# Performance work log

Measured on AMD Instinct MI355X. Metric: run time of the kernel, lower is better.

## Reference

```python
import jax, jax.numpy as jnp
import numpy as np

B, S, T, D, H_HEADS = 2, 2048, 2048, 1024, 16
HD = D // H_HEADS
EPS = 1e-5


def _ln(x, g, b):
    m = jnp.mean(x, axis=-1, keepdims=True)
    v = jnp.mean(jnp.square(x - m), axis=-1, keepdims=True)
    return g * (x - m) * jax.lax.rsqrt(v + EPS) + b


def _mha(xq, xkv, Wq, bq, Wk, bk, Wv, bv, Wo, bo, causal):
    Bq, Lq, _ = xq.shape
    Lk = xkv.shape[1]
    q = (xq @ Wq + bq).reshape(Bq, Lq, H_HEADS, HD)
    k = (xkv @ Wk + bk).reshape(Bq, Lk, H_HEADS, HD)
    v = (xkv @ Wv + bv).reshape(Bq, Lk, H_HEADS, HD)
    scores = jnp.einsum('bqhd,bkhd->bhqk', q, k) / jnp.sqrt(jnp.asarray(HD, q.dtype))
    if causal:
        mask = jnp.tril(jnp.ones((Lq, Lk), dtype=bool))
        scores = jnp.where(mask, scores, jnp.asarray(-1e9, scores.dtype))
    p = jax.nn.softmax(scores, axis=-1)
    o = jnp.einsum('bhqk,bkhd->bqhd', p, v).reshape(Bq, Lq, D)
    return o @ Wo + bo


def setup_inputs() -> dict:
    key = jax.random.key(0)
    ks = jax.random.split(key, 24)
    s = 0.02
    def w(i):
        return jax.random.normal(ks[i], (D, D), jnp.float32) * s
    inp = {
        'S0': jax.random.normal(ks[20], (B, S, D), jnp.float32),
        'H': jax.random.normal(ks[21], (B, T, D), jnp.float32),
        'Wq1': w(0), 'bq1': jnp.zeros((D,)), 'Wk1': w(1), 'bk1': jnp.zeros((D,)),
        'Wv1': w(2), 'bv1': jnp.zeros((D,)), 'Wo1': w(3), 'bo1': jnp.zeros((D,)),
        'ln1_g': jnp.ones((D,)), 'ln1_b': jnp.zeros((D,)),
        'Wq2': w(4), 'bq2': jnp.zeros((D,)), 'Wk2': w(5), 'bk2': jnp.zeros((D,)),
        'Wv2': w(6), 'bv2': jnp.zeros((D,)), 'Wo2': w(7), 'bo2': jnp.zeros((D,)),
        'ln2_g': jnp.ones((D,)), 'ln2_b': jnp.zeros((D,)),
        'Wf': w(8), 'bf': jnp.zeros((D,)),
        'ln3_g': jnp.ones((D,)), 'ln3_b': jnp.zeros((D,)),
    }
    return inp


def reference(S0, H, Wq1, bq1, Wk1, bk1, Wv1, bv1, Wo1, bo1, ln1_g, ln1_b,
              Wq2, bq2, Wk2, bk2, Wv2, bv2, Wo2, bo2, ln2_g, ln2_b,
              Wf, bf, ln3_g, ln3_b):
    # masked (causal) self-attention + add&norm
    a1 = _mha(S0, S0, Wq1, bq1, Wk1, bk1, Wv1, bv1, Wo1, bo1, causal=True)
    S1 = _ln(S0 + a1, ln1_g, ln1_b)
    # cross-attention over encoder output H + add&norm
    a2 = _mha(S1, H, Wq2, bq2, Wk2, bk2, Wv2, bv2, Wo2, bo2, causal=False)
    S2 = _ln(S1 + a2, ln2_g, ln2_b)
    # FFN (single Linear) + add&norm
    S3 = _ln(S2 + (S2 @ Wf + bf), ln3_g, ln3_b)
    return S3
```

## Files before the change

### kernel.cpp

```cpp
#include <hip/hip_runtime.h>
#include <hip/hip_bf16.h>
#include <cstdint>
#include <cstddef>


#define D_DIM 1024
#define SEQ   2048
#define NHEAD 16
#define HDIM  64
#define MROWS 4096

typedef __attribute__((ext_vector_type(8)))  short bf16x8;
typedef __attribute__((ext_vector_type(4)))  float f32x4;
typedef __attribute__((ext_vector_type(16))) float f32x16;
typedef __attribute__((ext_vector_type(4)))  unsigned int u32x4;

static __device__ __forceinline__ short f2bf(float x) {
    __hip_bfloat16 h = __float2bfloat16(x);
    return *reinterpret_cast<short*>(&h);
}

static __device__ __forceinline__ unsigned int cvtpk(float lo, float hi2) {
    unsigned int r;
    asm("v_cvt_pk_bf16_f32 %0, %1, %2" : "=v"(r) : "v"(lo), "v"(hi2));
    return r;
}

#define GLOAD_LDS16(g, l)                                                     \
    __builtin_amdgcn_global_load_lds(                                         \
        (const __attribute__((address_space(1))) unsigned int*)(g),           \
        (__attribute__((address_space(3))) unsigned int*)(l), 16, 0, 0)

struct WPtrs { const float* p[9]; };

__global__ __launch_bounds__(256) void transpose_conv_kernel(
    WPtrs wp, short* __restrict__ Wt)
{
    __shared__ float tl[64][65];
    const int t = threadIdx.x;
    const float* src = wp.p[blockIdx.z];
    short* dst = Wt + (size_t)blockIdx.z * D_DIM * D_DIM;
    const int r0 = blockIdx.x * 64;
    const int c0 = blockIdx.y * 64;
    #pragma unroll
    for (int i = 0; i < 4; ++i) {
        int row = i * 16 + (t >> 4);
        int col = (t & 15) * 4;
        float4 v = *(const float4*)(src + (size_t)(r0 + row) * D_DIM + c0 + col);
        tl[row][col + 0] = v.x; tl[row][col + 1] = v.y;
        tl[row][col + 2] = v.z; tl[row][col + 3] = v.w;
    }
    __syncthreads();
    #pragma unroll
    for (int i = 0; i < 4; ++i) {
        int nrow = i * 16 + (t >> 4);
        int kcol = (t & 15) * 4;
        ushort4 o;
        o.x = (unsigned short)f2bf(tl[kcol + 0][nrow]);
        o.y = (unsigned short)f2bf(tl[kcol + 1][nrow]);
        o.z = (unsigned short)f2bf(tl[kcol + 2][nrow]);
        o.w = (unsigned short)f2bf(tl[kcol + 3][nrow]);
        *(ushort4*)(dst + (size_t)(c0 + nrow) * D_DIM + r0 + kcol) = o;
    }
}

__global__ __launch_bounds__(256) void conv2_kernel(
    const float* __restrict__ s0, const float* __restrict__ hx,
    short* __restrict__ d0, short* __restrict__ d1)
{
    const bool second = blockIdx.x >= 2048;
    const float* src = second ? hx : s0;
    short* dst = second ? d1 : d0;
    size_t i = ((size_t)(blockIdx.x - (second ? 2048 : 0)) * 256 + threadIdx.x) * 8;
    float4 a = *(const float4*)(src + i);
    float4 b = *(const float4*)(src + i + 4);
    bf16x8 o;
    o[0] = f2bf(a.x); o[1] = f2bf(a.y); o[2] = f2bf(a.z); o[3] = f2bf(a.w);
    o[4] = f2bf(b.x); o[5] = f2bf(b.y); o[6] = f2bf(b.z); o[7] = f2bf(b.w);
    *(bf16x8*)(dst + i) = o;
}

__global__ __launch_bounds__(256) void bias_concat_kernel(
    const float* __restrict__ bq1, const float* __restrict__ bk1,
    const float* __restrict__ bv1, const float* __restrict__ bk2,
    const float* __restrict__ bv2, float* __restrict__ cb1,
    float* __restrict__ cb2)
{
    const int i = blockIdx.x * 256 + threadIdx.x;
    if      (i < 1024) cb1[i] = bq1[i];
    else if (i < 2048) cb1[i] = bk1[i - 1024];
    else if (i < 3072) cb1[i] = bv1[i - 2048];
    else if (i < 4096) cb2[i - 3072] = bk2[i - 3072];
    else               cb2[i - 3072] = bv2[i - 4096];
}

#define GEMM_CORE(A_, Bt_)                                                    \
    __shared__ short As[128 * 32];                                            \
    __shared__ short Bs[128 * 32];                                            \
    const int t = threadIdx.x;                                                \
    const int wave = t >> 6, lane = t & 63;                                   \
    const int wm = wave >> 1, wn = wave & 1;                                  \
    const int m0 = blockIdx.x * 128, n0 = blockIdx.y * 128;                   \
    const int l15 = lane & 15, l4 = lane >> 4;                                \
    const int lrow = lane >> 2, lcol = (lane & 3) * 8;                        \
    f32x4 acc[4][4] = {};                                                     \
    for (int k0 = 0; k0 < D_DIM; k0 += 32) {                                  \
        __syncthreads();                                                      \
        _Pragma("unroll")                                                     \
        for (int c = 0; c < 2; ++c) {                                         \
            int chunk = wave + c * 4;                                         \
            int row = chunk * 16 + lrow;                                      \
            GLOAD_LDS16(A_  + (size_t)(m0 + row) * D_DIM + k0 + lcol,         \
                        As + chunk * 512 + lane * 8);                         \
            GLOAD_LDS16(Bt_ + (size_t)(n0 + row) * D_DIM + k0 + lcol,         \
                        Bs + chunk * 512 + lane * 8);                         \
        }                                                                     \
        __syncthreads();                                                      \
        bf16x8 af[4], bfr[4];                                                 \
        const int kq = l4 * 8;                                                \
        _Pragma("unroll")                                                     \
        for (int i = 0; i < 4; ++i)                                           \
            af[i] = *(const bf16x8*)&As[(wm * 64 + i * 16 + l15) * 32 + kq];  \
        _Pragma("unroll")                                                     \
        for (int j = 0; j < 4; ++j)                                           \
            bfr[j] = *(const bf16x8*)&Bs[(wn * 64 + j * 16 + l15) * 32 + kq]; \
        _Pragma("unroll")                                                     \
        for (int i = 0; i < 4; ++i)                                           \
            _Pragma("unroll")                                                 \
            for (int j = 0; j < 4; ++j)                                       \
                acc[i][j] = __builtin_amdgcn_mfma_f32_16x16x32_bf16(          \
                    af[i], bfr[j], acc[i][j], 0, 0, 0);                       \
    }                                                                         \
    const int rbase = m0 + wm * 64;                                           \
    const int cbase = n0 + wn * 64;

__global__ __launch_bounds__(256) void gemm_resid_kernel(
    const short* __restrict__ A, const short* __restrict__ Bt,
    const float* __restrict__ bias, const float* __restrict__ resid,
    float* __restrict__ Cout)
{
    __shared__ short As[128 * 32];
    __shared__ short Bs[64 * 32];
    const int t = threadIdx.x;
    const int wave = t >> 6, lane = t & 63;
    const int wm = wave >> 1, wn = wave & 1;
    const int m0 = blockIdx.x * 128, n0 = blockIdx.y * 64;
    const int l15 = lane & 15, l4 = lane >> 4;
    const int lrow = lane >> 2, lcol = (lane & 3) * 8;
    f32x4 acc[4][2] = {};
    for (int k0 = 0; k0 < D_DIM; k0 += 32) {
        __syncthreads();
        #pragma unroll
        for (int c = 0; c < 2; ++c) {
            int chunk = wave + c * 4;
            int row = chunk * 16 + lrow;
            GLOAD_LDS16(A + (size_t)(m0 + row) * D_DIM + k0 + lcol,
                        As + chunk * 512 + lane * 8);
        }
        {
            int row = wave * 16 + lrow;
            GLOAD_LDS16(Bt + (size_t)(n0 + row) * D_DIM + k0 + lcol,
                        Bs + wave * 512 + lane * 8);
        }
        __syncthreads();
        bf16x8 af[4], bfr[2];
        const int kq = l4 * 8;
        #pragma unroll
        for (int i = 0; i < 4; ++i)
            af[i] = *(const bf16x8*)&As[(wm * 64 + i * 16 + l15) * 32 + kq];
        #pragma unroll
        for (int j = 0; j < 2; ++j)
            bfr[j] = *(const bf16x8*)&Bs[(wn * 32 + j * 16 + l15) * 32 + kq];
        #pragma unroll
        for (int i = 0; i < 4; ++i)
            #pragma unroll
            for (int j = 0; j < 2; ++j)
                acc[i][j] = __builtin_amdgcn_mfma_f32_16x16x32_bf16(
                    af[i], bfr[j], acc[i][j], 0, 0, 0);
    }
    const int rbase = m0 + wm * 64;
    const int cbase = n0 + wn * 32;
    float bv[2];
    #pragma unroll
    for (int j = 0; j < 2; ++j) bv[j] = bias[cbase + j * 16 + l15];
    #pragma unroll
    for (int i = 0; i < 4; ++i) {
        #pragma unroll
        for (int r = 0; r < 4; ++r) {
            const int grow = rbase + i * 16 + l4 * 4 + r;
            #pragma unroll
            for (int j = 0; j < 2; ++j) {
                const int gcol = cbase + j * 16 + l15;
                float v = acc[i][j][r] + bv[j]
                        + resid[(size_t)grow * D_DIM + gcol];
                Cout[(size_t)grow * D_DIM + gcol] = v;
            }
        }
    }
}

__global__ __launch_bounds__(256) void gemm_qkv_kernel(
    const short* __restrict__ A, const short* __restrict__ Bt,
    const float* __restrict__ bias,
    short* __restrict__ Qh, short* __restrict__ Kh, short* __restrict__ Vh,
    int col0, float qscale)
{
    GEMM_CORE(A, Bt)
    float bv[4];
    #pragma unroll
    for (int j = 0; j < 4; ++j) bv[j] = bias[cbase + j * 16 + l15];
    #pragma unroll
    for (int i = 0; i < 4; ++i) {
        #pragma unroll
        for (int r = 0; r < 4; ++r) {
            const int grow = rbase + i * 16 + l4 * 4 + r;
            const int b = grow >> 11, s = grow & 2047;
            #pragma unroll
            for (int j = 0; j < 4; ++j) {
                const int vcol = col0 + cbase + j * 16 + l15;
                float v = acc[i][j][r] + bv[j];
                if (vcol < 1024) v *= qscale;
                short* dst = (vcol < 1024) ? Qh : ((vcol < 2048) ? Kh : Vh);
                const int h = (vcol >> 6) & 15, hd = vcol & 63;
                dst[((size_t)(b * 16 + h) * SEQ + s) * HDIM + hd] = f2bf(v);
            }
        }
    }
}

template<bool CAUSAL>
__global__ __launch_bounds__(256, 2) void attn_mfma_kernel(
    const short* __restrict__ Qh, const short* __restrict__ Kh,
    const short* __restrict__ Vh, short* __restrict__ O)
{
    __shared__ short Ks[2][128 * 64];
    __shared__ short Vt[2][64 * 128];

    const int t = threadIdx.x, wave = t >> 6, lane = t & 63;
    const int q_own = lane & 31, hi = lane >> 5;
    const int id = blockIdx.x;
    const int bh = ((id & 7) << 2) | ((id >> 3) & 3);
    const int qsel = id >> 5;
    const int b = bh >> 4, h = bh & 15;
    const short* Qp = Qh + (size_t)bh * SEQ * HDIM;
    const short* Kp = Kh + (size_t)bh * SEQ * HDIM;
    const short* Vp = Vh + (size_t)bh * SEQ * HDIM;
    short* Op = O + (size_t)b * SEQ * D_DIM + h * HDIM;

    const int ksrc = (t & 7) ^ ((t >> 3) & 7);
    const int vr2 = (t & 31) * 2, vg = (t >> 5) * 8;

    bf16x8 va0, vb0, va1, vb1;

    #define K_GLL(kb, buf)                                                    \
        do {                                                                  \
            _Pragma("unroll")                                                 \
            for (int c = 0; c < 4; ++c) {                                     \
                const int row = c * 32 + (t >> 3);                            \
                GLOAD_LDS16(Kp + (size_t)((kb) + row) * HDIM + ksrc * 8,      \
                            &Ks[buf][(c * 256 + t) * 8]);                     \
            }                                                                 \
        } while (0)

    #define V_LOAD(kb)                                                        \
        do {                                                                  \
            va0 = *(const bf16x8*)(Vp + (size_t)((kb) + vr2) * HDIM + vg);    \
            vb0 = *(const bf16x8*)(Vp + (size_t)((kb) + vr2 + 1) * HDIM + vg);\
            va1 = *(const bf16x8*)(Vp + (size_t)((kb) + 64 + vr2) * HDIM + vg);\
            vb1 = *(const bf16x8*)(Vp + (size_t)((kb) + 64 + vr2 + 1) * HDIM + vg);\
        } while (0)

    #define V_WRITE(buf)                                                      \
        do {                                                                  \
            _Pragma("unroll")                                                 \
            for (int j = 0; j < 8; ++j) {                                     \
                const int hd = vg + j;                                        \
                unsigned int p0 = ((unsigned int)(unsigned short)vb0[j] << 16)\
                                | (unsigned short)va0[j];                     \
                *(unsigned int*)&Vt[buf][(hd * 128 + vr2) ^ ((hd & 7) << 3)] = p0;\
                unsigned int p1 = ((unsigned int)(unsigned short)vb1[j] << 16)\
                                | (unsigned short)va1[j];                     \
                *(unsigned int*)&Vt[buf][(hd * 128 + 64 + vr2) ^ ((hd & 7) << 3)] = p1;\
            }                                                                 \
        } while (0)

    const int npm = CAUSAL ? 2 : 1;
    for (int pm = 0; pm < npm; ++pm) {
        const int qt = CAUSAL ? (pm == 0 ? qsel : 15 - qsel) : qsel;
        const int q0 = qt * 128;
        const int qw = q0 + wave * 32;

        bf16x8 qf[4];
        #pragma unroll
        for (int s = 0; s < 4; ++s)
            qf[s] = *(const bf16x8*)(Qp + (size_t)(qw + q_own) * HDIM
                                     + s * 16 + hi * 8);

        f32x16 oacc[2] = {};
        float m_ = -3e38f, l_ = 0.f;
        const int nkt = CAUSAL ? (qt + 1) : (SEQ / 128);

        if (pm) __syncthreads();

        K_GLL(0, 0);
        V_LOAD(0);
        V_WRITE(0);
        __syncthreads();

        for (int kt = 0; kt < nkt; ++kt) {
            const int cur = kt & 1, nxt = cur ^ 1;
            const int kbase = kt * 128;
            const bool have_next = (kt + 1 < nkt);

            if (have_next) {
                K_GLL(kbase + 128, nxt);
                V_LOAD(kbase + 128);
            }

            f32x16 sc[4] = {};
            __builtin_amdgcn_s_setprio(1);
            #pragma unroll
            for (int kt2 = 0; kt2 < 4; ++kt2) {
                const int krow = kt2 * 32 + q_own;
                #pragma unroll
                for (int s = 0; s < 4; ++s) {
                    bf16x8 kf = *(const bf16x8*)&Ks[cur]
                        [(krow * 64 + s * 16 + hi * 8) ^ ((krow & 7) << 3)];
                    sc[kt2] = __builtin_amdgcn_mfma_f32_32x32x16_bf16(
                        kf, qf[s], sc[kt2], 0, 0, 0);
                }
            }
            __builtin_amdgcn_s_setprio(0);

            if (CAUSAL && (kbase + 127 > qw)) {
                #pragma unroll
                for (int kt2 = 0; kt2 < 4; ++kt2)
                    #pragma unroll
                    for (int rr = 0; rr < 16; ++rr) {
                        const int k = kbase + kt2 * 32
                                    + (rr & 3) + 8 * (rr >> 2) + 4 * hi;
                        if (k > qw + q_own) sc[kt2][rr] = -1e30f;
                    }
            }

            float pmax = sc[0][0];
            #pragma unroll
            for (int kt2 = 0; kt2 < 4; ++kt2) {
                float p0 = fmaxf(fmaxf(sc[kt2][0], sc[kt2][1]),
                                 fmaxf(sc[kt2][2], sc[kt2][3]));
                float p1 = fmaxf(fmaxf(sc[kt2][4], sc[kt2][5]),
                                 fmaxf(sc[kt2][6], sc[kt2][7]));
                float p2 = fmaxf(fmaxf(sc[kt2][8], sc[kt2][9]),
                                 fmaxf(sc[kt2][10], sc[kt2][11]));
                float p3 = fmaxf(fmaxf(sc[kt2][12], sc[kt2][13]),
                                 fmaxf(sc[kt2][14], sc[kt2][15]));
                float q01 = fmaxf(p0, p1), q23 = fmaxf(p2, p3);
                pmax = (kt2 == 0) ? fmaxf(q01, q23)
                                  : fmaxf(pmax, fmaxf(q01, q23));
            }
            pmax = fmaxf(pmax, __shfl_xor(pmax, 32));

            if (!__all(pmax - m_ <= 8.0f)) {
                const float mnew = fmaxf(m_, pmax);
                const float corr = exp2f(m_ - mnew);
                l_ *= corr;
                #pragma unroll
                for (int ht = 0; ht < 2; ++ht)
                    #pragma unroll
                    for (int rr = 0; rr < 16; ++rr)
                        oacc[ht][rr] *= corr;
                m_ = mnew;
            }

            float s_own = 0.f;
            #pragma unroll
            for (int kt2 = 0; kt2 < 4; ++kt2) {
                float t0 = 0.f, t1 = 0.f, t2 = 0.f, t3 = 0.f;
                #pragma unroll
                for (int rr = 0; rr < 4; ++rr) {
                    float a = exp2f(sc[kt2][rr]      - m_);
                    float b2 = exp2f(sc[kt2][4 + rr]  - m_);
                    float c = exp2f(sc[kt2][8 + rr]  - m_);
                    float d = exp2f(sc[kt2][12 + rr] - m_);
                    sc[kt2][rr] = a;      t0 += a;
                    sc[kt2][4 + rr] = b2; t1 += b2;
                    sc[kt2][8 + rr] = c;  t2 += c;
                    sc[kt2][12 + rr] = d; t3 += d;
                }
                s_own += (t0 + t1) + (t2 + t3);
            }
            l_ += s_own + __shfl_xor(s_own, 32);

            u32x4 paw[8];
            #pragma unroll
            for (int kt2 = 0; kt2 < 4; ++kt2) {
                unsigned int w0a = cvtpk(sc[kt2][0],  sc[kt2][1]);
                unsigned int w0b = cvtpk(sc[kt2][2],  sc[kt2][3]);
                unsigned int w1a = cvtpk(sc[kt2][4],  sc[kt2][5]);
                unsigned int w1b = cvtpk(sc[kt2][6],  sc[kt2][7]);
                unsigned int w2a = cvtpk(sc[kt2][8],  sc[kt2][9]);
                unsigned int w2b = cvtpk(sc[kt2][10], sc[kt2][11]);
                unsigned int w3a = cvtpk(sc[kt2][12], sc[kt2][13]);
                unsigned int w3b = cvtpk(sc[kt2][14], sc[kt2][15]);
                asm("v_permlane32_swap_b32 %0, %1" : "+v"(w0a), "+v"(w1a));
                asm("v_permlane32_swap_b32 %0, %1" : "+v"(w0b), "+v"(w1b));
                asm("v_permlane32_swap_b32 %0, %1" : "+v"(w2a), "+v"(w3a));
                asm("v_permlane32_swap_b32 %0, %1" : "+v"(w2b), "+v"(w3b));
                paw[kt2 * 2 + 0][0] = w0a; paw[kt2 * 2 + 0][1] = w0b;
                paw[kt2 * 2 + 0][2] = w1a; paw[kt2 * 2 + 0][3] = w1b;
                paw[kt2 * 2 + 1][0] = w2a; paw[kt2 * 2 + 1][1] = w2b;
                paw[kt2 * 2 + 1][2] = w3a; paw[kt2 * 2 + 1][3] = w3b;
            }

            __builtin_amdgcn_s_setprio(1);
            #pragma unroll
            for (int ht = 0; ht < 2; ++ht) {
                const int vrow = ht * 32 + q_own;
                #pragma unroll
                for (int ks = 0; ks < 8; ++ks) {
                    bf16x8 vf = *(const bf16x8*)&Vt[cur]
                        [(vrow * 128 + ks * 16 + hi * 8) ^ ((vrow & 7) << 3)];
                    union { u32x4 u; bf16x8 bv8; } pc;
                    pc.u = paw[ks];
                    oacc[ht] = __builtin_amdgcn_mfma_f32_32x32x16_bf16(
                        vf, pc.bv8, oacc[ht], 0, 0, 0);
                }
            }
            __builtin_amdgcn_s_setprio(0);

            if (have_next) {
                V_WRITE(nxt);
                __syncthreads();
            }
        }

        const float inv = 1.0f / l_;
        const int grow = qw + q_own;
        #pragma unroll
        for (int ht = 0; ht < 2; ++ht)
            #pragma unroll
            for (int j = 0; j < 4; ++j) {
                ushort4 o;
                o.x = (unsigned short)f2bf(oacc[ht][4 * j + 0] * inv);
                o.y = (unsigned short)f2bf(oacc[ht][4 * j + 1] * inv);
                o.z = (unsigned short)f2bf(oacc[ht][4 * j + 2] * inv);
                o.w = (unsigned short)f2bf(oacc[ht][4 * j + 3] * inv);
                *(ushort4*)&Op[(size_t)grow * D_DIM + ht * 32 + 8 * j + 4 * hi] = o;
            }
    }
    #undef K_GLL
    #undef V_LOAD
    #undef V_WRITE
}

__global__ __launch_bounds__(256) void ln_kernel(
    const float* __restrict__ X, const float* __restrict__ g,
    const float* __restrict__ bb, float* __restrict__ outf,
    short* __restrict__ outb)
{
    const int row = blockIdx.x;
    const int t = threadIdx.x;
    const float* x = X + (size_t)row * D_DIM;
    float4 v = *(const float4*)(x + (t << 2));
    float s  = v.x + v.y + v.z + v.w;
    float sq = v.x * v.x + v.y * v.y + v.z * v.z + v.w * v.w;
    #pragma unroll
    for (int off = 1; off < 64; off <<= 1) {
        s  += __shfl_xor(s, off);
        sq += __shfl_xor(sq, off);
    }
    __shared__ float ss[4], ssq[4];
    const int wid = t >> 6, lane = t & 63;
    if (lane == 0) { ss[wid] = s; ssq[wid] = sq; }
    __syncthreads();
    s  = ss[0] + ss[1] + ss[2] + ss[3];
    sq = ssq[0] + ssq[1] + ssq[2] + ssq[3];
    const float mean = s * (1.0f / 1024.0f);
    const float var  = sq * (1.0f / 1024.0f) - mean * mean;
    const float inv  = rsqrtf(var + 1e-5f);
    float4 gv = *(const float4*)(g  + (t << 2));
    float4 bv = *(const float4*)(bb + (t << 2));
    float4 o;
    o.x = gv.x * (v.x - mean) * inv + bv.x;
    o.y = gv.y * (v.y - mean) * inv + bv.y;
    o.z = gv.z * (v.z - mean) * inv + bv.z;
    o.w = gv.w * (v.w - mean) * inv + bv.w;
    if (outf) *(float4*)(outf + (size_t)row * D_DIM + (t << 2)) = o;
    if (outb) {
        ushort4 ob;
        ob.x = (unsigned short)f2bf(o.x); ob.y = (unsigned short)f2bf(o.y);
        ob.z = (unsigned short)f2bf(o.z); ob.w = (unsigned short)f2bf(o.w);
        *(ushort4*)(outb + (size_t)row * D_DIM + (t << 2)) = ob;
    }
}

extern "C" void kernel_launch(void* const* d_in, const int* in_sizes, int n_in,
                              void* d_out, int out_size, void* d_ws, size_t ws_size,
                              hipStream_t stream)
{
    (void)in_sizes; (void)n_in; (void)out_size; (void)ws_size;
    const float* S0f = (const float*)d_in[0];
    const float* Hf  = (const float*)d_in[1];
    const float* bq1 = (const float*)d_in[3];
    const float* bk1 = (const float*)d_in[5];
    const float* bv1 = (const float*)d_in[7];
    const float* bo1 = (const float*)d_in[9];
    const float* g1  = (const float*)d_in[10]; const float* b1 = (const float*)d_in[11];
    const float* bq2 = (const float*)d_in[13];
    const float* bk2 = (const float*)d_in[15];
    const float* bv2 = (const float*)d_in[17];
    const float* bo2 = (const float*)d_in[19];
    const float* g2  = (const float*)d_in[20]; const float* b2 = (const float*)d_in[21];
    const float* bff = (const float*)d_in[23];
    const float* g3  = (const float*)d_in[24]; const float* b3 = (const float*)d_in[25];

    char* ws = (char*)d_ws;
    size_t off = 0;
    auto alloc = [&](size_t bytes) { char* p = ws + off; off += (bytes + 255) & ~(size_t)255; return p; };
    short* Wt   = (short*)alloc((size_t)9 * D_DIM * D_DIM * 2);
    short* bS0  = (short*)alloc((size_t)MROWS * D_DIM * 2);
    short* bH   = (short*)alloc((size_t)MROWS * D_DIM * 2);
    short* Qhb  = (short*)alloc((size_t)MROWS * D_DIM * 2);
    short* Khb  = (short*)alloc((size_t)MROWS * D_DIM * 2);
    short* Vhb  = (short*)alloc((size_t)MROWS * D_DIM * 2);
    short* bAO  = (short*)alloc((size_t)MROWS * D_DIM * 2);
    float* X    = (float*)alloc((size_t)MROWS * D_DIM * 4);
    short* bSx  = (short*)alloc((size_t)MROWS * D_DIM * 2);
    float* cb1  = (float*)alloc(3072 * 4);
    float* cb2  = (float*)alloc(2048 * 4);

    const size_t WSTRIDE = (size_t)D_DIM * D_DIM;
    const float QSCALE = 0.125f * 1.44269504088896f;

    WPtrs wp;
    wp.p[0] = (const float*)d_in[2];
    wp.p[1] = (const float*)d_in[4];
    wp.p[2] = (const float*)d_in[6];
    wp.p[3] = (const float*)d_in[8];
    wp.p[4] = (const float*)d_in[12];
    wp.p[5] = (const float*)d_in[14];
    wp.p[6] = (const float*)d_in[16];
    wp.p[7] = (const float*)d_in[18];
    wp.p[8] = (const float*)d_in[22];
    transpose_conv_kernel<<<dim3(16, 16, 9), 256, 0, stream>>>(wp, Wt);

    conv2_kernel<<<4096, 256, 0, stream>>>(S0f, Hf, bS0, bH);
    bias_concat_kernel<<<20, 256, 0, stream>>>(bq1, bk1, bv1, bk2, bv2, cb1, cb2);

    const dim3 blk(256);
    const dim3 attn_grid_c(256);
    const dim3 attn_grid_f(512);
    const dim3 resid_grid(32, 16);

    gemm_qkv_kernel<<<dim3(32, 24), blk, 0, stream>>>(
        bS0, Wt, cb1, Qhb, Khb, Vhb, 0, QSCALE);
    attn_mfma_kernel<true><<<attn_grid_c, blk, 0, stream>>>(Qhb, Khb, Vhb, bAO);
    gemm_resid_kernel<<<resid_grid, blk, 0, stream>>>(
        bAO, Wt + 3 * WSTRIDE, bo1, S0f, X);
    ln_kernel<<<MROWS, blk, 0, stream>>>(X, g1, b1, X, bSx);

    gemm_qkv_kernel<<<dim3(32, 8), blk, 0, stream>>>(
        bSx, Wt + 4 * WSTRIDE, bq2, Qhb, Khb, Vhb, 0, QSCALE);
    gemm_qkv_kernel<<<dim3(32, 16), blk, 0, stream>>>(
        bH, Wt + 5 * WSTRIDE, cb2, Qhb, Khb, Vhb, 1024, QSCALE);
    attn_mfma_kernel<false><<<attn_grid_f, blk, 0, stream>>>(Qhb, Khb, Vhb, bAO);
    gemm_resid_kernel<<<resid_grid, blk, 0, stream>>>(
        bAO, Wt + 7 * WSTRIDE, bo2, X, X);
    ln_kernel<<<MROWS, blk, 0, stream>>>(X, g2, b2, X, bSx);

    gemm_resid_kernel<<<resid_grid, blk, 0, stream>>>(
        bSx, Wt + 8 * WSTRIDE, bff, X, X);
    ln_kernel<<<MROWS, blk, 0, stream>>>(X, g3, b3, (float*)d_out, nullptr);
}
```

Before: 302.5 us.

## Fuse cross-attention K/V projection into causal attention launch to fill idle CUs

The cross-attention K/V projection of H does not depend on the first attention block, so it is moved into the same launch as the causal self-attention: blocks 0-255 run attention and blocks 256-767 run the K/V GEMM into separate Kh2/Vh2 buffers. This is meant to fill compute units left idle by the 256-block causal attention grid and its load imbalance, and it removes one launch. In exchange, two extra workspace buffers are allocated, and the GEMM blocks now carry the attention kernel's 64KB LDS footprint and launch bounds, which can lower their occupancy.

Result: faster. 281.3 us (-7.0%).

```diff
diff --git a/kernel.cpp b/kernel.cpp
--- a/kernel.cpp
+++ b/kernel.cpp
@@ -94,45 +94,81 @@
     else               cb2[i - 3072] = bv2[i - 4096];
 }
 
-#define GEMM_CORE(A_, Bt_)                                                    \
-    __shared__ short As[128 * 32];                                            \
-    __shared__ short Bs[128 * 32];                                            \
-    const int t = threadIdx.x;                                                \
-    const int wave = t >> 6, lane = t & 63;                                   \
-    const int wm = wave >> 1, wn = wave & 1;                                  \
-    const int m0 = blockIdx.x * 128, n0 = blockIdx.y * 128;                   \
-    const int l15 = lane & 15, l4 = lane >> 4;                                \
-    const int lrow = lane >> 2, lcol = (lane & 3) * 8;                        \
-    f32x4 acc[4][4] = {};                                                     \
-    for (int k0 = 0; k0 < D_DIM; k0 += 32) {                                  \
-        __syncthreads();                                                      \
-        _Pragma("unroll")                                                     \
-        for (int c = 0; c < 2; ++c) {                                         \
-            int chunk = wave + c * 4;                                         \
-            int row = chunk * 16 + lrow;                                      \
-            GLOAD_LDS16(A_  + (size_t)(m0 + row) * D_DIM + k0 + lcol,         \
-                        As + chunk * 512 + lane * 8);                         \
-            GLOAD_LDS16(Bt_ + (size_t)(n0 + row) * D_DIM + k0 + lcol,         \
-                        Bs + chunk * 512 + lane * 8);                         \
-        }                                                                     \
-        __syncthreads();                                                      \
-        bf16x8 af[4], bfr[4];                                                 \
-        const int kq = l4 * 8;                                                \
-        _Pragma("unroll")                                                     \
-        for (int i = 0; i < 4; ++i)                                           \
-            af[i] = *(const bf16x8*)&As[(wm * 64 + i * 16 + l15) * 32 + kq];  \
-        _Pragma("unroll")                                                     \
-        for (int j = 0; j < 4; ++j)                                           \
-            bfr[j] = *(const bf16x8*)&Bs[(wn * 64 + j * 16 + l15) * 32 + kq]; \
-        _Pragma("unroll")                                                     \
-        for (int i = 0; i < 4; ++i)                                           \
-            _Pragma("unroll")                                                 \
-            for (int j = 0; j < 4; ++j)                                       \
-                acc[i][j] = __builtin_amdgcn_mfma_f32_16x16x32_bf16(          \
-                    af[i], bfr[j], acc[i][j], 0, 0, 0);                       \
-    }                                                                         \
-    const int rbase = m0 + wm * 64;                                           \
+__device__ __forceinline__ void gemm_qkv_body(
+    short* __restrict__ As_, short* __restrict__ Bs_,
+    const short* __restrict__ A, const short* __restrict__ Bt,
+    const float* __restrict__ bias,
+    short* __restrict__ Qh, short* __restrict__ Kh, short* __restrict__ Vh,
+    int col0, float qscale, int bx, int by)
+{
+    const int t = threadIdx.x;
+    const int wave = t >> 6, lane = t & 63;
+    const int wm = wave >> 1, wn = wave & 1;
+    const int m0 = bx * 128, n0 = by * 128;
+    const int l15 = lane & 15, l4 = lane >> 4;
+    const int lrow = lane >> 2, lcol = (lane & 3) * 8;
+    f32x4 acc[4][4] = {};
+    for (int k0 = 0; k0 < D_DIM; k0 += 32) {
+        __syncthreads();
+        #pragma unroll
+        for (int c = 0; c < 2; ++c) {
+            int chunk = wave + c * 4;
+            int row = chunk * 16 + lrow;
+            GLOAD_LDS16(A  + (size_t)(m0 + row) * D_DIM + k0 + lcol,
+                        As_ + chunk * 512 + lane * 8);
+            GLOAD_LDS16(Bt + (size_t)(n0 + row) * D_DIM + k0 + lcol,
+                        Bs_ + chunk * 512 + lane * 8);
+        }
+        __syncthreads();
+        bf16x8 af[4], bfr[4];
+        const int kq = l4 * 8;
+        #pragma unroll
+        for (int i = 0; i < 4; ++i)
+            af[i] = *(const bf16x8*)&As_[(wm * 64 + i * 16 + l15) * 32 + kq];
+        #pragma unroll
+        for (int j = 0; j < 4; ++j)
+            bfr[j] = *(const bf16x8*)&Bs_[(wn * 64 + j * 16 + l15) * 32 + kq];
+        #pragma unroll
+        for (int i = 0; i < 4; ++i)
+            #pragma unroll
+            for (int j = 0; j < 4; ++j)
+                acc[i][j] = __builtin_amdgcn_mfma_f32_16x16x32_bf16(
+                    af[i], bfr[j], acc[i][j], 0, 0, 0);
+    }
+    const int rbase = m0 + wm * 64;
     const int cbase = n0 + wn * 64;
+    float bv[4];
+    #pragma unroll
+    for (int j = 0; j < 4; ++j) bv[j] = bias[cbase + j * 16 + l15];
+    #pragma unroll
+    for (int i = 0; i < 4; ++i) {
+        #pragma unroll
+        for (int r = 0; r < 4; ++r) {
+            const int grow = rbase + i * 16 + l4 * 4 + r;
+            const int b = grow >> 11, s = grow & 2047;
+            #pragma unroll
+            for (int j = 0; j < 4; ++j) {
+                const int vcol = col0 + cbase + j * 16 + l15;
+                float v = acc[i][j][r] + bv[j];
+                if (vcol < 1024) v *= qscale;
+                short* dst = (vcol < 1024) ? Qh : ((vcol < 2048) ? Kh : Vh);
+                const int h = (vcol >> 6) & 15, hd = vcol & 63;
+                dst[((size_t)(b * 16 + h) * SEQ + s) * HDIM + hd] = f2bf(v);
+            }
+        }
+    }
+}
+
+__global__ __launch_bounds__(256) void gemm_qkv_kernel(
+    const short* __restrict__ A, const short* __restrict__ Bt,
+    const float* __restrict__ bias,
+    short* __restrict__ Qh, short* __restrict__ Kh, short* __restrict__ Vh,
+    int col0, float qscale)
+{
+    __shared__ short lds[8192];
+    gemm_qkv_body(lds, lds + 4096, A, Bt, bias, Qh, Kh, Vh,
+                  col0, qscale, blockIdx.x, blockIdx.y);
+}
 
 __global__ __launch_bounds__(256) void gemm_resid_kernel(
     const short* __restrict__ A, const short* __restrict__ Bt,
@@ -199,46 +235,14 @@
     }
 }
 
-__global__ __launch_bounds__(256) void gemm_qkv_kernel(
-    const short* __restrict__ A, const short* __restrict__ Bt,
-    const float* __restrict__ bias,
-    short* __restrict__ Qh, short* __restrict__ Kh, short* __restrict__ Vh,
-    int col0, float qscale)
-{
-    GEMM_CORE(A, Bt)
-    float bv[4];
-    #pragma unroll
-    for (int j = 0; j < 4; ++j) bv[j] = bias[cbase + j * 16 + l15];
-    #pragma unroll
-    for (int i = 0; i < 4; ++i) {
-        #pragma unroll
-        for (int r = 0; r < 4; ++r) {
-            const int grow = rbase + i * 16 + l4 * 4 + r;
-            const int b = grow >> 11, s = grow & 2047;
-            #pragma unroll
-            for (int j = 0; j < 4; ++j) {
-                const int vcol = col0 + cbase + j * 16 + l15;
-                float v = acc[i][j][r] + bv[j];
-                if (vcol < 1024) v *= qscale;
-                short* dst = (vcol < 1024) ? Qh : ((vcol < 2048) ? Kh : Vh);
-                const int h = (vcol >> 6) & 15, hd = vcol & 63;
-                dst[((size_t)(b * 16 + h) * SEQ + s) * HDIM + hd] = f2bf(v);
-            }
-        }
-    }
-}
-
 template<bool CAUSAL>
-__global__ __launch_bounds__(256, 2) void attn_mfma_kernel(
+__device__ __forceinline__ void attn_body(
+    short* __restrict__ KsB, short* __restrict__ VtB,
     const short* __restrict__ Qh, const short* __restrict__ Kh,
-    const short* __restrict__ Vh, short* __restrict__ O)
-{
-    __shared__ short Ks[2][128 * 64];
-    __shared__ short Vt[2][64 * 128];
-
+    const short* __restrict__ Vh, short* __restrict__ O, const int id)
+{
     const int t = threadIdx.x, wave = t >> 6, lane = t & 63;
     const int q_own = lane & 31, hi = lane >> 5;
-    const int id = blockIdx.x;
     const int bh = ((id & 7) << 2) | ((id >> 3) & 3);
     const int qsel = id >> 5;
     const int b = bh >> 4, h = bh & 15;
@@ -258,7 +262,7 @@
             for (int c = 0; c < 4; ++c) {                                     \
                 const int row = c * 32 + (t >> 3);                            \
                 GLOAD_LDS16(Kp + (size_t)((kb) + row) * HDIM + ksrc * 8,      \
-                            &Ks[buf][(c * 256 + t) * 8]);                     \
+                            KsB + (buf) * 8192 + (c * 256 + t) * 8);          \
             }                                                                 \
         } while (0)
 
@@ -277,10 +281,12 @@
                 const int hd = vg + j;                                        \
                 unsigned int p0 = ((unsigned int)(unsigned short)vb0[j] << 16)\
                                 | (unsigned short)va0[j];                     \
-                *(unsigned int*)&Vt[buf][(hd * 128 + vr2) ^ ((hd & 7) << 3)] = p0;\
+                *(unsigned int*)&VtB[(buf) * 8192                             \
+                    + ((hd * 128 + vr2) ^ ((hd & 7) << 3))] = p0;             \
                 unsigned int p1 = ((unsigned int)(unsigned short)vb1[j] << 16)\
                                 | (unsigned short)va1[j];                     \
-                *(unsigned int*)&Vt[buf][(hd * 128 + 64 + vr2) ^ ((hd & 7) << 3)] = p1;\
+                *(unsigned int*)&VtB[(buf) * 8192                             \
+                    + ((hd * 128 + 64 + vr2) ^ ((hd & 7) << 3))] = p1;        \
             }                                                                 \
         } while (0)
 
@@ -324,8 +330,8 @@
                 const int krow = kt2 * 32 + q_own;
                 #pragma unroll
                 for (int s = 0; s < 4; ++s) {
-                    bf16x8 kf = *(const bf16x8*)&Ks[cur]
-                        [(krow * 64 + s * 16 + hi * 8) ^ ((krow & 7) << 3)];
+                    bf16x8 kf = *(const bf16x8*)&KsB[cur * 8192
+                        + ((krow * 64 + s * 16 + hi * 8) ^ ((krow & 7) << 3))];
                     sc[kt2] = __builtin_amdgcn_mfma_f32_32x32x16_bf16(
                         kf, qf[s], sc[kt2], 0, 0, 0);
                 }
@@ -378,10 +384,10 @@
                 float t0 = 0.f, t1 = 0.f, t2 = 0.f, t3 = 0.f;
                 #pragma unroll
                 for (int rr = 0; rr < 4; ++rr) {
-                    float a = exp2f(sc[kt2][rr]      - m_);
+                    float a  = exp2f(sc[kt2][rr]      - m_);
                     float b2 = exp2f(sc[kt2][4 + rr]  - m_);
-                    float c = exp2f(sc[kt2][8 + rr]  - m_);
-                    float d = exp2f(sc[kt2][12 + rr] - m_);
+                    float c  = exp2f(sc[kt2][8 + rr]  - m_);
+                    float d  = exp2f(sc[kt2][12 + rr] - m_);
                     sc[kt2][rr] = a;      t0 += a;
                     sc[kt2][4 + rr] = b2; t1 += b2;
                     sc[kt2][8 + rr] = c;  t2 += c;
@@ -418,8 +424,8 @@
                 const int vrow = ht * 32 + q_own;
                 #pragma unroll
                 for (int ks = 0; ks < 8; ++ks) {
-                    bf16x8 vf = *(const bf16x8*)&Vt[cur]
-                        [(vrow * 128 + ks * 16 + hi * 8) ^ ((vrow & 7) << 3)];
+                    bf16x8 vf = *(const bf16x8*)&VtB[cur * 8192
+                        + ((vrow * 128 + ks * 16 + hi * 8) ^ ((vrow & 7) << 3))];
                     union { u32x4 u; bf16x8 bv8; } pc;
                     pc.u = paw[ks];
                     oacc[ht] = __builtin_amdgcn_mfma_f32_32x32x16_bf16(
@@ -451,6 +457,32 @@
     #undef K_GLL
     #undef V_LOAD
     #undef V_WRITE
+}
+
+template<bool CAUSAL>
+__global__ __launch_bounds__(256, 2) void attn_mfma_kernel(
+    const short* __restrict__ Qh, const short* __restrict__ Kh,
+    const short* __restrict__ Vh, short* __restrict__ O)
+{
+    __shared__ short lds[32768];
+    attn_body<CAUSAL>(lds, lds + 16384, Qh, Kh, Vh, O, blockIdx.x);
+}
+
+__global__ __launch_bounds__(256, 2) void fused_cattn_kv2_kernel(
+    const short* __restrict__ Qh, const short* __restrict__ Kh,
+    const short* __restrict__ Vh, short* __restrict__ O,
+    const short* __restrict__ A2, const short* __restrict__ Bt2,
+    const float* __restrict__ bias2,
+    short* __restrict__ Kh2, short* __restrict__ Vh2)
+{
+    __shared__ short lds[32768];
+    if (blockIdx.x < 256) {
+        attn_body<true>(lds, lds + 16384, Qh, Kh, Vh, O, blockIdx.x);
+    } else {
+        const int bx2 = blockIdx.x - 256;
+        gemm_qkv_body(lds, lds + 4096, A2, Bt2, bias2,
+                      nullptr, Kh2, Vh2, 1024, 1.0f, bx2 & 31, bx2 >> 5);
+    }
 }
 
 __global__ __launch_bounds__(256) void ln_kernel(
@@ -523,6 +555,8 @@
     short* Qhb  = (short*)alloc((size_t)MROWS * D_DIM * 2);
     short* Khb  = (short*)alloc((size_t)MROWS * D_DIM * 2);
     short* Vhb  = (short*)alloc((size_t)MROWS * D_DIM * 2);
+    short* Khb2 = (short*)alloc((size_t)MROWS * D_DIM * 2);
+    short* Vhb2 = (short*)alloc((size_t)MROWS * D_DIM * 2);
     short* bAO  = (short*)alloc((size_t)MROWS * D_DIM * 2);
     float* X    = (float*)alloc((size_t)MROWS * D_DIM * 4);
     short* bSx  = (short*)alloc((size_t)MROWS * D_DIM * 2);
@@ -548,22 +582,21 @@
     bias_concat_kernel<<<20, 256, 0, stream>>>(bq1, bk1, bv1, bk2, bv2, cb1, cb2);
 
     const dim3 blk(256);
-    const dim3 attn_grid_c(256);
     const dim3 attn_grid_f(512);
     const dim3 resid_grid(32, 16);
 
     gemm_qkv_kernel<<<dim3(32, 24), blk, 0, stream>>>(
         bS0, Wt, cb1, Qhb, Khb, Vhb, 0, QSCALE);
-    attn_mfma_kernel<true><<<attn_grid_c, blk, 0, stream>>>(Qhb, Khb, Vhb, bAO);
+    fused_cattn_kv2_kernel<<<dim3(768), blk, 0, stream>>>(
+        Qhb, Khb, Vhb, bAO, bH, Wt + 5 * WSTRIDE, cb2, Khb2, Vhb2);
     gemm_resid_kernel<<<resid_grid, blk, 0, stream>>>(
         bAO, Wt + 3 * WSTRIDE, bo1, S0f, X);
     ln_kernel<<<MROWS, blk, 0, stream>>>(X, g1, b1, X, bSx);
 
     gemm_qkv_kernel<<<dim3(32, 8), blk, 0, stream>>>(
         bSx, Wt + 4 * WSTRIDE, bq2, Qhb, Khb, Vhb, 0, QSCALE);
-    gemm_qkv_kernel<<<dim3(32, 16), blk, 0, stream>>>(
-        bH, Wt + 5 * WSTRIDE, cb2, Qhb, Khb, Vhb, 1024, QSCALE);
-    attn_mfma_kernel<false><<<attn_grid_f, blk, 0, stream>>>(Qhb, Khb, Vhb, bAO);
+    attn_mfma_kernel<false><<<attn_grid_f, blk, 0, stream>>>(
+        Qhb, Khb2, Vhb2, bAO);
     gemm_resid_kernel<<<resid_grid, blk, 0, stream>>>(
         bAO, Wt + 7 * WSTRIDE, bo2, X, X);
     ln_kernel<<<MROWS, blk, 0, stream>>>(X, g2, b2, X, bSx);
```
